# Optimization experiments

Measured on AMD Instinct MI355X. Metric: run time of the kernel, lower is better.

Reference implementation:

```python
import jax, jax.numpy as jnp
import numpy as np

N, C, H, W = 8, 256, 28, 28
K = 64
EPS = 1e-12  # F.normalize eps
BN_EPS = 1e-5


def setup_inputs() -> dict:
    key = jax.random.key(0)
    k1, k2, k3 = jax.random.split(key, 3)
    x = jax.random.normal(k1, (N, C, H, W), dtype=jnp.float32)
    conv_w = jax.random.normal(k2, (K, C), dtype=jnp.float32) * 0.05  # 1x1 conv, no bias (vlad_v2=False)
    centroids = jax.random.uniform(k3, (K, C), dtype=jnp.float32)    # torch.rand init
    bn_w = jnp.ones((K * C,), dtype=jnp.float32)
    bn_b = jnp.zeros((K * C,), dtype=jnp.float32)
    return {"x": x, "conv_w": conv_w, "centroids": centroids, "bn_w": bn_w, "bn_b": bn_b}


def _l2norm(v, axis):
    n = jnp.sqrt(jnp.sum(v * v, axis=axis, keepdims=True))
    return v / jnp.maximum(n, EPS)


def reference(x, conv_w, centroids, bn_w, bn_b):
    n, c, h, w = x.shape
    k = centroids.shape[0]
    P = h * w
    # descriptor-wise L2 normalize over channels
    xn = _l2norm(x, axis=1)
    xf = xn.reshape(n, c, P)                                   # (N, C, P)
    # 1x1 conv soft assignment + softmax over clusters
    soft_assign = jnp.einsum('ncp,kc->nkp', xf, conv_w)        # (N, K, P)
    soft_assign = jax.nn.softmax(soft_assign, axis=1)
    # weighted residuals (N, K, C, P)
    residual = (xf[:, None, :, :] - centroids[None, :, :, None]) * soft_assign[:, :, None, :]
    # intra-normalize over flattened (K*C) per spatial location
    rn = jnp.sqrt(jnp.sum(residual * residual, axis=(1, 2), keepdims=True))  # (N,1,1,P)
    residual = residual / jnp.maximum(rn, EPS)
    # sum pool over spatial, then per-cluster L2 normalize over C
    vlad = residual.sum(axis=-1)                               # (N, K, C)
    vlad = _l2norm(vlad, axis=2)
    v = vlad.reshape(n, k * c)
    # BatchNorm1d in training mode: batch stats, biased variance
    mean = jnp.mean(v, axis=0)
    var = jnp.var(v, axis=0)
    v = (v - mean) / jnp.sqrt(var + BN_EPS) * bn_w + bn_b
    # final L2 normalize
    return _l2norm(v, axis=1)
```

## Files before the change

### kernel.cpp

```cpp
#include <hip/hip_runtime.h>
#include <math.h>

#define N_ 8
#define C_ 256
#define P_ 784
#define K_ 64
#define F_ 16384
#define FEPS 1e-12f
#define BNEPS 1e-5f
#define PBLK 25

__device__ __forceinline__ float wave_sum(float v) {
#pragma unroll
  for (int s = 1; s < 64; s <<= 1) v += __shfl_xor(v, s, 64);
  return v;
}
__device__ __forceinline__ float wave_max(float v) {
#pragma unroll
  for (int s = 1; s < 64; s <<= 1) v = fmaxf(v, __shfl_xor(v, s, 64));
  return v;
}

__global__ __launch_bounds__(512) void k_fused1(const float* __restrict__ x,
                                                const float* __restrict__ convw,
                                                const float* __restrict__ cent,
                                                float* __restrict__ w2,
                                                float* __restrict__ Spart) {
  __shared__ float As[2][128][36];
  __shared__ float G_lds[128][34];
  __shared__ float w2_lds[64][36];
  __shared__ float cn2p[64][9];
  __shared__ float cn2_lds[64];
  __shared__ float rinv_lds[32];
  __shared__ float xn2_lds[32];
  __shared__ float sp_lds[8][65];

  const int pblk = blockIdx.x, n = blockIdx.y;
  const int p0 = pblk * 32;
  const int t = threadIdx.x;
  const int wv = t >> 6, lane = t & 63;
  const float* xb = x + (size_t)n * C_ * P_;

  const int tx = t & 15, ty = t >> 4;
  const int scc = t & 31, skg = t >> 5;
  const int pbase = p0 + tx * 2;
  const float* xcol = xb + ((pbase + 1 < P_) ? pbase : (P_ - 2));

  {
    int k = t >> 3, oct = t & 7;
    const float* row = cent + (size_t)k * C_ + oct * 32;
    float s = 0.f;
#pragma unroll
    for (int i = 0; i < 8; ++i) {
      float4 v = *(const float4*)&row[i * 4];
      s += v.x * v.x + v.y * v.y + v.z * v.z + v.w * v.w;
    }
    cn2p[k][oct] = s;
  }
#pragma unroll
  for (int i = 0; i < 8; ++i) {
    int kk = skg * 8 + i;
    const float* Ar = (kk < 64) ? (convw + (size_t)kk * C_) : (cent + (size_t)(kk - 64) * C_);
    As[0][kk][scc] = Ar[scc];
  }
  __syncthreads();
  if (t < 64) {
    float s = 0.f;
#pragma unroll
    for (int i = 0; i < 8; ++i) s += cn2p[t][i];
    cn2_lds[t] = s;
  }

  float acc[4][2] = {};
  float ssq0 = 0.f, ssq1 = 0.f;

  for (int ch = 0; ch < 8; ++ch) {
    const int cur = ch & 1;
    const int c0 = ch * 32;
    float anext[8];
    if (ch < 7) {
      int c0n = c0 + 32;
#pragma unroll
      for (int i = 0; i < 8; ++i) {
        int kk = skg * 8 + i;
        const float* Ar = (kk < 64) ? (convw + (size_t)kk * C_) : (cent + (size_t)(kk - 64) * C_);
        anext[i] = Ar[c0n + scc];
      }
    }
    const float* xc = xcol + (size_t)c0 * P_;
#pragma unroll
    for (int cc4 = 0; cc4 < 32; cc4 += 4) {
      float2 xv0 = *(const float2*)&xc[(size_t)(cc4 + 0) * P_];
      float2 xv1 = *(const float2*)&xc[(size_t)(cc4 + 1) * P_];
      float2 xv2 = *(const float2*)&xc[(size_t)(cc4 + 2) * P_];
      float2 xv3 = *(const float2*)&xc[(size_t)(cc4 + 3) * P_];
      float4 a0 = *(const float4*)&As[cur][ty * 4 + 0][cc4];
      float4 a1 = *(const float4*)&As[cur][ty * 4 + 1][cc4];
      float4 a2 = *(const float4*)&As[cur][ty * 4 + 2][cc4];
      float4 a3 = *(const float4*)&As[cur][ty * 4 + 3][cc4];
      float xa[4] = {xv0.x, xv1.x, xv2.x, xv3.x};
      float xbv[4] = {xv0.y, xv1.y, xv2.y, xv3.y};
      float av[4][4] = {{a0.x, a0.y, a0.z, a0.w},
                        {a1.x, a1.y, a1.z, a1.w},
                        {a2.x, a2.y, a2.z, a2.w},
                        {a3.x, a3.y, a3.z, a3.w}};
#pragma unroll
      for (int i = 0; i < 4; ++i)
#pragma unroll
        for (int j = 0; j < 4; ++j) {
          acc[i][0] += av[i][j] * xa[j];
          acc[i][1] += av[i][j] * xbv[j];
        }
      if (wv == 0) {
#pragma unroll
        for (int j = 0; j < 4; ++j) { ssq0 += xa[j] * xa[j]; ssq1 += xbv[j] * xbv[j]; }
      }
    }
    if (ch < 7) {
      const int nxt = cur ^ 1;
#pragma unroll
      for (int i = 0; i < 8; ++i) As[nxt][skg * 8 + i][scc] = anext[i];
    }
    __syncthreads();
  }

#pragma unroll
  for (int i = 0; i < 4; ++i)
    *(float2*)&G_lds[ty * 4 + i][tx * 2] = make_float2(acc[i][0], acc[i][1]);
  if (t < 16) {
    float r0 = 1.0f / fmaxf(sqrtf(ssq0), FEPS);
    float r1 = 1.0f / fmaxf(sqrtf(ssq1), FEPS);
    rinv_lds[tx * 2] = r0;
    rinv_lds[tx * 2 + 1] = r1;
    xn2_lds[tx * 2] = ssq0 * r0 * r0;
    xn2_lds[tx * 2 + 1] = ssq1 * r1 * r1;
  }
  __syncthreads();

  float s_acc = 0.f;
  float c2 = cn2_lds[lane];
#pragma unroll
  for (int j = 0; j < 4; ++j) {
    int pl = wv * 4 + j;
    if (p0 + pl < P_) {
      float r = rinv_lds[pl];
      float x2 = xn2_lds[pl];
      float lg = G_lds[lane][pl] * r;
      float dt = G_lds[64 + lane][pl] * r;
      float m = wave_max(lg);
      float e = expf(lg - m);
      float ssum = wave_sum(e);
      float a = e / ssum;
      float rn2 = wave_sum(a * a * (x2 - 2.f * dt + c2));
      float wf = 1.0f / fmaxf(sqrtf(rn2), FEPS);
      float wval = a * wf;
      s_acc += wval;
      w2_lds[lane][pl] = wval * r;
    }
  }
  sp_lds[wv][lane] = s_acc;
  __syncthreads();
  if (t < 64) {
    float s = 0.f;
#pragma unroll
    for (int g = 0; g < 8; ++g) s += sp_lds[g][t];
    Spart[((size_t)pblk * N_ + n) * 64 + t] = s;
  }
  {
    int k = t >> 3, q = t & 7;
    int p = p0 + q * 4;
    if (p + 3 < P_) {
      float4 v = *(const float4*)&w2_lds[k][q * 4];
      *(float4*)&w2[((size_t)n * K_ + k) * P_ + p] = v;
    }
  }
}

__global__ __launch_bounds__(256) void k_gemm2(const float* __restrict__ x,
                                               const float* __restrict__ w2,
                                               float* __restrict__ vpart) {
  __shared__ float WsT[32][68];
  __shared__ float XsT[32][68];
  int n = blockIdx.z, s = blockIdx.y;
  int c0 = blockIdx.x * 64;
  int t = threadIdx.x;
  int tx = t & 15, ty = t >> 4;
  float acc[4][4] = {};
  const float* wb = w2 + (size_t)n * K_ * P_;
  const float* xb = x + (size_t)n * C_ * P_;
  int pbase = s * 98;
  for (int q = 0; q < 98; q += 32) {
    int r = t >> 5, pc = t & 31;
    bool ok = (q + pc) < 98;
    int p = pbase + q + pc;
#pragma unroll
    for (int i = 0; i < 8; ++i) {
      int row = r + i * 8;
      WsT[pc][row] = ok ? wb[(size_t)row * P_ + p] : 0.f;
      XsT[pc][row] = ok ? xb[(size_t)(c0 + row) * P_ + p] : 0.f;
    }
    __syncthreads();
#pragma unroll
    for (int pp = 0; pp < 32; ++pp) {
      float4 a = *(const float4*)&WsT[pp][ty * 4];
      float4 bv = *(const float4*)&XsT[pp][tx * 4];
      float av[4] = {a.x, a.y, a.z, a.w};
      float bb[4] = {bv.x, bv.y, bv.z, bv.w};
#pragma unroll
      for (int i = 0; i < 4; ++i)
#pragma unroll
        for (int j = 0; j < 4; ++j) acc[i][j] += av[i] * bb[j];
    }
    __syncthreads();
  }
  float* vb = vpart + (size_t)(s * N_ + n) * K_ * C_;
#pragma unroll
  for (int i = 0; i < 4; ++i)
#pragma unroll
    for (int j = 0; j < 4; ++j)
      vb[(size_t)(ty * 4 + i) * C_ + c0 + tx * 4 + j] = acc[i][j];
}

__global__ __launch_bounds__(256) void k_vladnorm(const float* __restrict__ vpart,
                                                  const float* __restrict__ cent,
                                                  const float* __restrict__ Spart,
                                                  float* __restrict__ vladn) {
  __shared__ float red[4];
  int b = blockIdx.x;
  int n = b >> 6, k = b & 63;
  int c = threadIdx.x;
  float Sb = 0.f;
#pragma unroll
  for (int s = 0; s < PBLK; ++s) Sb += Spart[((size_t)s * N_ + n) * 64 + k];
  float val = 0.f;
#pragma unroll
  for (int s = 0; s < 8; ++s) val += vpart[(size_t)(s * 512 + b) * C_ + c];
  val -= cent[(size_t)k * C_ + c] * Sb;
  float ss = wave_sum(val * val);
  int wv = threadIdx.x >> 6, lane = threadIdx.x & 63;
  if (lane == 0) red[wv] = ss;
  __syncthreads();
  float tot = red[0] + red[1] + red[2] + red[3];
  float inv = 1.0f / fmaxf(sqrtf(tot), FEPS);
  vladn[(size_t)b * C_ + c] = val * inv;
}

__global__ __launch_bounds__(256) void k_bn(const float* __restrict__ vladn,
                                            const float* __restrict__ bnw,
                                            const float* __restrict__ bnb,
                                            float* __restrict__ ybuf,
                                            float* __restrict__ nrmpart) {
  __shared__ float red[4][8];
  int f = blockIdx.x * 256 + threadIdx.x;
  float v[N_];
  float s = 0.f;
#pragma unroll
  for (int n = 0; n < N_; ++n) { v[n] = vladn[(size_t)n * F_ + f]; s += v[n]; }
  float mean = s * (1.0f / N_);
  float s2 = 0.f;
#pragma unroll
  for (int n = 0; n < N_; ++n) { float d = v[n] - mean; s2 += d * d; }
  float var = s2 * (1.0f / N_);
  float sc = bnw[f] / sqrtf(var + BNEPS);
  float bb = bnb[f];
  float y[N_];
#pragma unroll
  for (int n = 0; n < N_; ++n) {
    y[n] = (v[n] - mean) * sc + bb;
    ybuf[(size_t)n * F_ + f] = y[n];
  }
  int wv = threadIdx.x >> 6, lane = threadIdx.x & 63;
#pragma unroll
  for (int n = 0; n < N_; ++n) {
    float q = wave_sum(y[n] * y[n]);
    if (lane == 0) red[wv][n] = q;
  }
  __syncthreads();
  if (threadIdx.x < N_) {
    int n = threadIdx.x;
    nrmpart[n * 64 + blockIdx.x] = red[0][n] + red[1][n] + red[2][n] + red[3][n];
  }
}

__global__ __launch_bounds__(256) void k_final(const float* __restrict__ ybuf,
                                               const float* __restrict__ nrmpart,
                                               float* __restrict__ out) {
  int idx = blockIdx.x * 256 + threadIdx.x;
  int n = idx >> 14;
  float tot = 0.f;
#pragma unroll
  for (int b = 0; b < 64; ++b) tot += nrmpart[n * 64 + b];
  float inv = 1.0f / fmaxf(sqrtf(tot), FEPS);
  out[idx] = ybuf[idx] * inv;
}

extern "C" void kernel_launch(void* const* d_in, const int* in_sizes, int n_in,
                              void* d_out, int out_size, void* d_ws, size_t ws_size,
                              hipStream_t stream) {
  const float* x = (const float*)d_in[0];
  const float* convw = (const float*)d_in[1];
  const float* cent = (const float*)d_in[2];
  const float* bnw = (const float*)d_in[3];
  const float* bnb = (const float*)d_in[4];
  float* out = (float*)d_out;
  float* ws = (float*)d_ws;

  float* Spart = ws;
  float* nrmpart = ws + 12800;
  float* w2 = ws + 13312;
  float* vpart = ws + 414720;
  float* vladn = ws + 1463296;
  float* ybuf = ws + 1594368;

  k_fused1<<<dim3(PBLK, N_), 512, 0, stream>>>(x, convw, cent, w2, Spart);
  k_gemm2<<<dim3(4, 8, 8), 256, 0, stream>>>(x, w2, vpart);
  k_vladnorm<<<512, 256, 0, stream>>>(vpart, cent, Spart, vladn);
  k_bn<<<64, 256, 0, stream>>>(vladn, bnw, bnb, ybuf, nrmpart);
  k_final<<<512, 256, 0, stream>>>(ybuf, nrmpart, out);
}
```

Measured before the change: 61.58 us.

## Split channel reduction across two thread groups with transposed A tile in LDS

New measurement: 59.03 us. 4.1% less time.

```diff
diff --git a/kernel.cpp b/kernel.cpp
--- a/kernel.cpp
+++ b/kernel.cpp
@@ -26,25 +26,35 @@
                                                 const float* __restrict__ cent,
                                                 float* __restrict__ w2,
                                                 float* __restrict__ Spart) {
-  __shared__ float As[2][128][36];
+  __shared__ float AsT[32][136];
   __shared__ float G_lds[128][34];
-  __shared__ float w2_lds[64][36];
-  __shared__ float cn2p[64][9];
+  __shared__ float ubuf[64 * 36];
   __shared__ float cn2_lds[64];
+  __shared__ float ssq_ab[2][32];
   __shared__ float rinv_lds[32];
   __shared__ float xn2_lds[32];
   __shared__ float sp_lds[8][65];
+
+  float (*w2_lds)[36] = (float(*)[36])ubuf;
+  float (*cn2p)[9] = (float(*)[9])ubuf;
 
   const int pblk = blockIdx.x, n = blockIdx.y;
   const int p0 = pblk * 32;
   const int t = threadIdx.x;
   const int wv = t >> 6, lane = t & 63;
+  const int grp = t >> 8;
+  const int tl = t & 255;
+  const int ty = tl >> 3;
+  const int tx = tl & 7;
+  const int ccb = grp * 16;
   const float* xb = x + (size_t)n * C_ * P_;
 
-  const int tx = t & 15, ty = t >> 4;
-  const int scc = t & 31, skg = t >> 5;
-  const int pbase = p0 + tx * 2;
-  const float* xcol = xb + ((pbase + 1 < P_) ? pbase : (P_ - 2));
+  int pj[4];
+#pragma unroll
+  for (int j = 0; j < 4; ++j) {
+    int p = p0 + tx + 8 * j;
+    pj[j] = (p < P_) ? p : 0;
+  }
 
   {
     int k = t >> 3, oct = t & 7;
@@ -57,83 +67,84 @@
     }
     cn2p[k][oct] = s;
   }
+  const int scc = t & 31, sk = t >> 5;
 #pragma unroll
   for (int i = 0; i < 8; ++i) {
-    int kk = skg * 8 + i;
+    int kk = sk * 8 + i;
     const float* Ar = (kk < 64) ? (convw + (size_t)kk * C_) : (cent + (size_t)(kk - 64) * C_);
-    As[0][kk][scc] = Ar[scc];
-  }
-  __syncthreads();
-  if (t < 64) {
-    float s = 0.f;
-#pragma unroll
-    for (int i = 0; i < 8; ++i) s += cn2p[t][i];
-    cn2_lds[t] = s;
-  }
-
-  float acc[4][2] = {};
-  float ssq0 = 0.f, ssq1 = 0.f;
+    AsT[scc][kk] = Ar[scc];
+  }
+  __syncthreads();
+
+  float acc[4][4] = {};
+  float ssqr[4] = {0.f, 0.f, 0.f, 0.f};
 
   for (int ch = 0; ch < 8; ++ch) {
-    const int cur = ch & 1;
     const int c0 = ch * 32;
     float anext[8];
     if (ch < 7) {
       int c0n = c0 + 32;
 #pragma unroll
       for (int i = 0; i < 8; ++i) {
-        int kk = skg * 8 + i;
+        int kk = sk * 8 + i;
         const float* Ar = (kk < 64) ? (convw + (size_t)kk * C_) : (cent + (size_t)(kk - 64) * C_);
         anext[i] = Ar[c0n + scc];
       }
     }
-    const float* xc = xcol + (size_t)c0 * P_;
-#pragma unroll
-    for (int cc4 = 0; cc4 < 32; cc4 += 4) {
-      float2 xv0 = *(const float2*)&xc[(size_t)(cc4 + 0) * P_];
-      float2 xv1 = *(const float2*)&xc[(size_t)(cc4 + 1) * P_];
-      float2 xv2 = *(const float2*)&xc[(size_t)(cc4 + 2) * P_];
-      float2 xv3 = *(const float2*)&xc[(size_t)(cc4 + 3) * P_];
-      float4 a0 = *(const float4*)&As[cur][ty * 4 + 0][cc4];
-      float4 a1 = *(const float4*)&As[cur][ty * 4 + 1][cc4];
-      float4 a2 = *(const float4*)&As[cur][ty * 4 + 2][cc4];
-      float4 a3 = *(const float4*)&As[cur][ty * 4 + 3][cc4];
-      float xa[4] = {xv0.x, xv1.x, xv2.x, xv3.x};
-      float xbv[4] = {xv0.y, xv1.y, xv2.y, xv3.y};
-      float av[4][4] = {{a0.x, a0.y, a0.z, a0.w},
-                        {a1.x, a1.y, a1.z, a1.w},
-                        {a2.x, a2.y, a2.z, a2.w},
-                        {a3.x, a3.y, a3.z, a3.w}};
+    if (ch == 0 && t < 64) {
+      float s = 0.f;
+#pragma unroll
+      for (int i = 0; i < 8; ++i) s += cn2p[t][i];
+      cn2_lds[t] = s;
+    }
+#pragma unroll
+    for (int cc = 0; cc < 16; ++cc) {
+      const float* xr = xb + (size_t)(c0 + ccb + cc) * P_;
+      float xv[4];
+#pragma unroll
+      for (int j = 0; j < 4; ++j) xv[j] = xr[pj[j]];
+      float4 a = *(const float4*)&AsT[ccb + cc][ty * 4];
+      if (ty == 0) {
+#pragma unroll
+        for (int j = 0; j < 4; ++j) ssqr[j] += xv[j] * xv[j];
+      }
+      float av[4] = {a.x, a.y, a.z, a.w};
 #pragma unroll
       for (int i = 0; i < 4; ++i)
 #pragma unroll
-        for (int j = 0; j < 4; ++j) {
-          acc[i][0] += av[i][j] * xa[j];
-          acc[i][1] += av[i][j] * xbv[j];
-        }
-      if (wv == 0) {
-#pragma unroll
-        for (int j = 0; j < 4; ++j) { ssq0 += xa[j] * xa[j]; ssq1 += xbv[j] * xbv[j]; }
-      }
-    }
+        for (int j = 0; j < 4; ++j) acc[i][j] += av[i] * xv[j];
+    }
+    __syncthreads();
     if (ch < 7) {
-      const int nxt = cur ^ 1;
-#pragma unroll
-      for (int i = 0; i < 8; ++i) As[nxt][skg * 8 + i][scc] = anext[i];
-    }
-    __syncthreads();
-  }
-
-#pragma unroll
-  for (int i = 0; i < 4; ++i)
-    *(float2*)&G_lds[ty * 4 + i][tx * 2] = make_float2(acc[i][0], acc[i][1]);
-  if (t < 16) {
-    float r0 = 1.0f / fmaxf(sqrtf(ssq0), FEPS);
-    float r1 = 1.0f / fmaxf(sqrtf(ssq1), FEPS);
-    rinv_lds[tx * 2] = r0;
-    rinv_lds[tx * 2 + 1] = r1;
-    xn2_lds[tx * 2] = ssq0 * r0 * r0;
-    xn2_lds[tx * 2 + 1] = ssq1 * r1 * r1;
+#pragma unroll
+      for (int i = 0; i < 8; ++i) AsT[scc][sk * 8 + i] = anext[i];
+      __syncthreads();
+    }
+  }
+
+  if (grp == 0) {
+#pragma unroll
+    for (int i = 0; i < 4; ++i)
+#pragma unroll
+      for (int j = 0; j < 4; ++j) G_lds[ty * 4 + i][tx + 8 * j] = acc[i][j];
+  }
+  if (ty == 0) {
+#pragma unroll
+    for (int j = 0; j < 4; ++j) ssq_ab[grp][tx + 8 * j] = ssqr[j];
+  }
+  __syncthreads();
+  if (grp == 1) {
+#pragma unroll
+    for (int i = 0; i < 4; ++i)
+#pragma unroll
+      for (int j = 0; j < 4; ++j) G_lds[ty * 4 + i][tx + 8 * j] += acc[i][j];
+  }
+  __syncthreads();
+  if (t < 32) {
+    float s = ssq_ab[0][t] + ssq_ab[1][t];
+    float r = 1.0f / fmaxf(sqrtf(s), FEPS);
+    rinv_lds[t] = r;
+    xn2_lds[t] = s * r * r;
   }
   __syncthreads();
 
```

## Restructure fused assignment GEMM to per-lane positions with wave-uniform weight rows

Applied to the files above, without the earlier changes.

New measurement: 93.47 us. 51.8% more time.

```diff
diff --git a/kernel.cpp b/kernel.cpp
--- a/kernel.cpp
+++ b/kernel.cpp
@@ -8,7 +8,7 @@
 #define F_ 16384
 #define FEPS 1e-12f
 #define BNEPS 1e-5f
-#define PBLK 25
+#define PBLK 13
 
 __device__ __forceinline__ float wave_sum(float v) {
 #pragma unroll
@@ -21,32 +21,31 @@
   return v;
 }
 
-__global__ __launch_bounds__(512) void k_fused1(const float* __restrict__ x,
-                                                const float* __restrict__ convw,
-                                                const float* __restrict__ cent,
-                                                float* __restrict__ w2,
-                                                float* __restrict__ Spart) {
-  __shared__ float As[2][128][36];
-  __shared__ float G_lds[128][34];
-  __shared__ float w2_lds[64][36];
-  __shared__ float cn2p[64][9];
+__global__ __launch_bounds__(1024) void k_fused1(const float* __restrict__ x,
+                                                 const float* __restrict__ convw,
+                                                 const float* __restrict__ cent,
+                                                 float* __restrict__ w2,
+                                                 float* __restrict__ Spart) {
+  __shared__ float G_lds[64][133];
+  __shared__ float w2u[64 * 68];
   __shared__ float cn2_lds[64];
-  __shared__ float rinv_lds[32];
-  __shared__ float xn2_lds[32];
-  __shared__ float sp_lds[8][65];
+  __shared__ float rinv_lds[64];
+  __shared__ float xn2_lds[64];
+  __shared__ float sp_lds[16][65];
+
+  float (*w2_lds)[68] = (float(*)[68])w2u;
+  float (*cn2p)[9] = (float(*)[9])w2u;
 
   const int pblk = blockIdx.x, n = blockIdx.y;
-  const int p0 = pblk * 32;
+  const int p0 = pblk * 64;
   const int t = threadIdx.x;
-  const int wv = t >> 6, lane = t & 63;
+  const int lane = t & 63;
+  const int wid = __builtin_amdgcn_readfirstlane(t >> 6);
   const float* xb = x + (size_t)n * C_ * P_;
-
-  const int tx = t & 15, ty = t >> 4;
-  const int scc = t & 31, skg = t >> 5;
-  const int pbase = p0 + tx * 2;
-  const float* xcol = xb + ((pbase + 1 < P_) ? pbase : (P_ - 2));
-
-  {
+  const int myp = p0 + lane;
+  const int xp = (myp < P_) ? myp : (P_ - 1);
+
+  if (t < 512) {
     int k = t >> 3, oct = t & 7;
     const float* row = cent + (size_t)k * C_ + oct * 32;
     float s = 0.f;
@@ -57,12 +56,6 @@
     }
     cn2p[k][oct] = s;
   }
-#pragma unroll
-  for (int i = 0; i < 8; ++i) {
-    int kk = skg * 8 + i;
-    const float* Ar = (kk < 64) ? (convw + (size_t)kk * C_) : (cent + (size_t)(kk - 64) * C_);
-    As[0][kk][scc] = Ar[scc];
-  }
   __syncthreads();
   if (t < 64) {
     float s = 0.f;
@@ -71,69 +64,51 @@
     cn2_lds[t] = s;
   }
 
-  float acc[4][2] = {};
-  float ssq0 = 0.f, ssq1 = 0.f;
+  const float* Arow = (wid < 8) ? (convw + (size_t)(wid * 8) * C_)
+                                : (cent + (size_t)(wid * 8 - 64) * C_);
+
+  float acc[8] = {0.f, 0.f, 0.f, 0.f, 0.f, 0.f, 0.f, 0.f};
+  float ssq = 0.f;
+  float xcur[32], xnxt[32];
+#pragma unroll
+  for (int cc = 0; cc < 32; ++cc) xcur[cc] = xb[(size_t)cc * P_ + xp];
 
   for (int ch = 0; ch < 8; ++ch) {
-    const int cur = ch & 1;
     const int c0 = ch * 32;
-    float anext[8];
     if (ch < 7) {
-      int c0n = c0 + 32;
-#pragma unroll
-      for (int i = 0; i < 8; ++i) {
-        int kk = skg * 8 + i;
-        const float* Ar = (kk < 64) ? (convw + (size_t)kk * C_) : (cent + (size_t)(kk - 64) * C_);
-        anext[i] = Ar[c0n + scc];
-      }
-    }
-    const float* xc = xcol + (size_t)c0 * P_;
-#pragma unroll
-    for (int cc4 = 0; cc4 < 32; cc4 += 4) {
-      float2 xv0 = *(const float2*)&xc[(size_t)(cc4 + 0) * P_];
-      float2 xv1 = *(const float2*)&xc[(size_t)(cc4 + 1) * P_];
-      float2 xv2 = *(const float2*)&xc[(size_t)(cc4 + 2) * P_];
-      float2 xv3 = *(const float2*)&xc[(size_t)(cc4 + 3) * P_];
-      float4 a0 = *(const float4*)&As[cur][ty * 4 + 0][cc4];
-      float4 a1 = *(const float4*)&As[cur][ty * 4 + 1][cc4];
-      float4 a2 = *(const float4*)&As[cur][ty * 4 + 2][cc4];
-      float4 a3 = *(const float4*)&As[cur][ty * 4 + 3][cc4];
-      float xa[4] = {xv0.x, xv1.x, xv2.x, xv3.x};
-      float xbv[4] = {xv0.y, xv1.y, xv2.y, xv3.y};
-      float av[4][4] = {{a0.x, a0.y, a0.z, a0.w},
-                        {a1.x, a1.y, a1.z, a1.w},
-                        {a2.x, a2.y, a2.z, a2.w},
-                        {a3.x, a3.y, a3.z, a3.w}};
-#pragma unroll
-      for (int i = 0; i < 4; ++i)
-#pragma unroll
-        for (int j = 0; j < 4; ++j) {
-          acc[i][0] += av[i][j] * xa[j];
-          acc[i][1] += av[i][j] * xbv[j];
-        }
-      if (wv == 0) {
-#pragma unroll
-        for (int j = 0; j < 4; ++j) { ssq0 += xa[j] * xa[j]; ssq1 += xbv[j] * xbv[j]; }
-      }
+#pragma unroll
+      for (int cc = 0; cc < 32; ++cc) xnxt[cc] = xb[(size_t)(c0 + 32 + cc) * P_ + xp];
+    }
+    if (wid == 0) {
+#pragma unroll
+      for (int cc = 0; cc < 32; ++cc) ssq = fmaf(xcur[cc], xcur[cc], ssq);
+    }
+#pragma unroll
+    for (int sl = 0; sl < 8; ++sl) {
+      float as[8][4];
+#pragma unroll
+      for (int i = 0; i < 8; ++i)
+#pragma unroll
+        for (int q = 0; q < 4; ++q)
+          as[i][q] = Arow[(size_t)i * C_ + c0 + sl * 4 + q];
+#pragma unroll
+      for (int q = 0; q < 4; ++q)
+#pragma unroll
+        for (int i = 0; i < 8; ++i)
+          acc[i] = fmaf(as[i][q], xcur[sl * 4 + q], acc[i]);
     }
     if (ch < 7) {
-      const int nxt = cur ^ 1;
-#pragma unroll
-      for (int i = 0; i < 8; ++i) As[nxt][skg * 8 + i][scc] = anext[i];
-    }
-    __syncthreads();
-  }
-
-#pragma unroll
-  for (int i = 0; i < 4; ++i)
-    *(float2*)&G_lds[ty * 4 + i][tx * 2] = make_float2(acc[i][0], acc[i][1]);
-  if (t < 16) {
-    float r0 = 1.0f / fmaxf(sqrtf(ssq0), FEPS);
-    float r1 = 1.0f / fmaxf(sqrtf(ssq1), FEPS);
-    rinv_lds[tx * 2] = r0;
-    rinv_lds[tx * 2 + 1] = r1;
-    xn2_lds[tx * 2] = ssq0 * r0 * r0;
-    xn2_lds[tx * 2 + 1] = ssq1 * r1 * r1;
+#pragma unroll
+      for (int cc = 0; cc < 32; ++cc) xcur[cc] = xnxt[cc];
+    }
+  }
+
+#pragma unroll
+  for (int i = 0; i < 8; ++i) G_lds[lane][wid * 8 + i] = acc[i];
+  if (wid == 0) {
+    float r = 1.0f / fmaxf(sqrtf(ssq), FEPS);
+    rinv_lds[lane] = r;
+    xn2_lds[lane] = ssq * r * r;
   }
   __syncthreads();
 
@@ -141,12 +116,12 @@
   float c2 = cn2_lds[lane];
 #pragma unroll
   for (int j = 0; j < 4; ++j) {
-    int pl = wv * 4 + j;
+    int pl = wid * 4 + j;
     if (p0 + pl < P_) {
       float r = rinv_lds[pl];
       float x2 = xn2_lds[pl];
-      float lg = G_lds[lane][pl] * r;
-      float dt = G_lds[64 + lane][pl] * r;
+      float lg = G_lds[pl][lane] * r;
+      float dt = G_lds[pl][64 + lane] * r;
       float m = wave_max(lg);
       float e = expf(lg - m);
       float ssum = wave_sum(e);
@@ -158,16 +133,16 @@
       w2_lds[lane][pl] = wval * r;
     }
   }
-  sp_lds[wv][lane] = s_acc;
+  sp_lds[wid][lane] = s_acc;
   __syncthreads();
   if (t < 64) {
     float s = 0.f;
 #pragma unroll
-    for (int g = 0; g < 8; ++g) s += sp_lds[g][t];
+    for (int g = 0; g < 16; ++g) s += sp_lds[g][t];
     Spart[((size_t)pblk * N_ + n) * 64 + t] = s;
   }
   {
-    int k = t >> 3, q = t & 7;
+    int k = t >> 4, q = t & 15;
     int p = p0 + q * 4;
     if (p + 3 < P_) {
       float4 v = *(const float4*)&w2_lds[k][q * 4];
@@ -306,13 +281,13 @@
   float* ws = (float*)d_ws;
 
   float* Spart = ws;
-  float* nrmpart = ws + 12800;
-  float* w2 = ws + 13312;
-  float* vpart = ws + 414720;
-  float* vladn = ws + 1463296;
-  float* ybuf = ws + 1594368;
-
-  k_fused1<<<dim3(PBLK, N_), 512, 0, stream>>>(x, convw, cent, w2, Spart);
+  float* nrmpart = ws + 6656;
+  float* w2 = ws + 7168;
+  float* vpart = ws + 408576;
+  float* vladn = ws + 1457152;
+  float* ybuf = ws + 1588224;
+
+  k_fused1<<<dim3(PBLK, N_), 1024, 0, stream>>>(x, convw, cent, w2, Spart);
   k_gemm2<<<dim3(4, 8, 8), 256, 0, stream>>>(x, w2, vpart);
   k_vladnorm<<<512, 256, 0, stream>>>(vpart, cent, Spart, vladn);
   k_bn<<<64, 256, 0, stream>>>(vladn, bnw, bnb, ybuf, nrmpart);
```
